# Kernel optimization log

Hardware: AMD Instinct MI355X
Metric: run time of the kernel (lower is better)

The kernel has to match this reference:

```python
import jax, jax.numpy as jnp
import numpy as np

S, B, H = 2048, 16, 512      # seq_len, batch, hidden_size
L = 4096                     # total labels across batch
SMAX = 16                    # max span length
LAB = 256                    # label_size
V = 32000                    # len(voc)


def setup_inputs() -> dict:
    key = jax.random.key(0)
    ks = jax.random.split(key, 10)
    hidden = jax.random.normal(ks[0], (S, B, H), jnp.float32)
    begins = jax.random.randint(ks[1], (L,), 1, S - SMAX - 1)          # >=1 so begin-1 valid
    lens = jax.random.randint(ks[2], (L,), 1, SMAX + 1)                # span length in [1, SMAX]
    ends = begins + lens                                               # < S so hidden[end] valid
    bids = jax.random.randint(ks[3], (L,), 0, B)
    tags = jax.random.randint(ks[4], (L,), 0, V)
    sc = 0.02
    W1 = jax.random.normal(ks[5], (3 * H, LAB), jnp.float32) * sc
    b1 = jnp.zeros((LAB,), jnp.float32)
    W2 = jax.random.normal(ks[6], (LAB, LAB), jnp.float32) * sc
    b2 = jnp.zeros((LAB,), jnp.float32)
    Wo = jax.random.normal(ks[7], (LAB, V), jnp.float32) * sc
    bo = jnp.zeros((V,), jnp.float32)
    return dict(hidden=hidden, begins=begins, ends=ends, bids=bids, tags=tags,
                W1=W1, b1=b1, W2=W2, b2=b2, Wo=Wo, bo=bo)


def reference(hidden, begins, ends, bids, tags, W1, b1, W2, b2, Wo, bo):
    # --- batched span embed: gather + masked mean + boundary concat ---
    pos = begins[:, None] + jnp.arange(SMAX)            # [L, SMAX]
    valid = (pos < ends[:, None]).astype(hidden.dtype)  # [L, SMAX]
    posc = jnp.minimum(pos, S - 1)
    g = hidden[posc, bids[:, None]]                     # [L, SMAX, H] gather
    span_len = (ends - begins).astype(hidden.dtype)[:, None]
    mean = (g * valid[..., None]).sum(axis=1) / span_len           # [L, H]
    left = hidden[begins - 1, bids]                                 # [L, H]
    right = hidden[ends, bids]                                      # [L, H]
    span_emb = jnp.concatenate([left, mean, right], axis=-1)        # [L, 3H]
    # --- hidden2feature: Linear -> sigmoid -> Linear (dropout = eval identity) ---
    feat = jax.nn.sigmoid(span_emb @ W1 + b1) @ W2 + b2             # [L, LAB]
    # --- SoftmaxLoss: -log_softmax(h2o(feat)).gather(tags).mean() per label ---
    logp = jax.nn.log_softmax(feat @ Wo + bo, axis=-1)              # [L, V]
    per_label = -logp[jnp.arange(L), tags]                          # one tag per label
    return per_label.sum() / (L + 1e-5)
```

## Files before the change

### kernel.cpp

```cpp
#include <hip/hip_runtime.h>
#include <math.h>

#define S 2048
#define B 16
#define H 512
#define L 4096
#define SMAX 16
#define LAB 256
#define V 32000
#define NCH 250
#define LOG2E 1.44269504f

typedef __attribute__((ext_vector_type(8))) short short8;
typedef __attribute__((ext_vector_type(4))) float float4v;

__device__ inline ushort f2bf(float x) {
  union { float f; unsigned u; } c; c.f = x;
  unsigned r = c.u + 0x7fffu + ((c.u >> 16) & 1u);
  return (ushort)(r >> 16);
}
__device__ inline float bf2f(ushort h) {
  union { unsigned u; float f; } c; c.u = ((unsigned)h) << 16;
  return c.f;
}

__global__ __launch_bounds__(256) void prep_kernel(
    const float* __restrict__ hidden, const int* __restrict__ begins,
    const int* __restrict__ ends, const int* __restrict__ bids,
    ushort* __restrict__ spanb, const float* __restrict__ W1,
    ushort* __restrict__ W1b, const float* __restrict__ W2,
    ushort* __restrict__ W2b, const float* __restrict__ Wo,
    ushort* __restrict__ Wob) {
  __shared__ ushort tile[64 * 72];
  int bid = blockIdx.x;
  int t = threadIdx.x;

  if (bid < 2048) {
    int sub = t >> 7, tt = t & 127;
    int l = bid * 2 + sub;
    int b = bids[l], s0 = begins[l], s1 = ends[l];
    const float4* hidv = (const float4*)hidden;
    float4 lf = hidv[((size_t)(s0 - 1) * B + b) * 128 + tt];
    float4 rf = hidv[((size_t)s1 * B + b) * 128 + tt];
    float4 m = make_float4(0.f, 0.f, 0.f, 0.f);
    int len = s1 - s0;
    for (int j = 0; j < len; ++j) {
      float4 g = hidv[((size_t)(s0 + j) * B + b) * 128 + tt];
      m.x += g.x; m.y += g.y; m.z += g.z; m.w += g.w;
    }
    float inv = 1.0f / (float)len;
    ushort* sp = spanb + (size_t)l * 1536;
    ushort4 u;
    u.x = f2bf(lf.x); u.y = f2bf(lf.y); u.z = f2bf(lf.z); u.w = f2bf(lf.w);
    *(ushort4*)&sp[tt * 4] = u;
    u.x = f2bf(m.x * inv); u.y = f2bf(m.y * inv);
    u.z = f2bf(m.z * inv); u.w = f2bf(m.w * inv);
    *(ushort4*)&sp[512 + tt * 4] = u;
    u.x = f2bf(rf.x); u.y = f2bf(rf.y); u.z = f2bf(rf.z); u.w = f2bf(rf.w);
    *(ushort4*)&sp[1024 + tt * 4] = u;
    return;
  }

  const float* src; ushort* dst; int K, N, n0, k0; bool wo = false;
  if (bid < 2144) {
    int u = bid - 2048; src = W1; dst = W1b; K = 1536; N = 256;
    n0 = (u & 3) * 64; k0 = (u >> 2) * 64;
  } else if (bid < 2160) {
    int u = bid - 2144; src = W2; dst = W2b; K = 256; N = 256;
    n0 = (u & 3) * 64; k0 = (u >> 2) * 64;
  } else {
    int u = bid - 2160; src = Wo; dst = Wob; K = 256; N = V;
    n0 = (u % 500) * 64; k0 = (u / 500) * 64; wo = true;
  }
  #pragma unroll
  for (int p = 0; p < 16; ++p) {
    int k = p * 4 + (t >> 6);
    int n = t & 63;
    tile[n * 72 + k] = f2bf(src[(size_t)(k0 + k) * N + n0 + n]);
  }
  __syncthreads();
  if (!wo) {
    #pragma unroll
    for (int p = 0; p < 2; ++p) {
      int idx = p * 256 + t;
      int n = idx >> 3, c = idx & 7;
      *(uint4*)&dst[(size_t)(n0 + n) * K + k0 + c * 8] =
          *(const uint4*)&tile[n * 72 + c * 8];
    }
  } else {
    #pragma unroll
    for (int p = 0; p < 2; ++p) {
      int idx = p * 256 + t;
      int n = idx >> 3, c8 = idx & 7;
      int v = n0 + n, k = k0 + c8 * 8;
      int c = v >> 7, nt = (v >> 4) & 7, lr = v & 15;
      int kh = k >> 7, k4 = (k >> 5) & 3, lq = (k >> 3) & 3;
      size_t f = ((((size_t)c * 2 + kh) * 4 + k4) * 8 + nt) * 64 + lq * 16 + lr;
      *(uint4*)&dst[f * 8] = *(const uint4*)&tile[n * 72 + c8 * 8];
    }
  }
}

__global__ __launch_bounds__(256) void feat_mfma_kernel(
    const ushort* __restrict__ spanb, const ushort* __restrict__ W1b,
    const float* __restrict__ b1, const ushort* __restrict__ W2b,
    const float* __restrict__ b2, ushort* __restrict__ featb,
    float* __restrict__ out) {
  __shared__ ushort Hs[16 * 264];
  int tid = threadIdx.x;
  if (blockIdx.x == 0 && tid == 0) *out = 0.f;
  int w = tid >> 6, lane = tid & 63;
  int lr = lane & 15, lq = lane >> 4;
  int l0 = blockIdx.x * 16;

  const short8* arow = (const short8*)(spanb + (size_t)(l0 + lr) * 1536 + lq * 8);
  const short8* brow[4];
  #pragma unroll
  for (int nt = 0; nt < 4; ++nt)
    brow[nt] = (const short8*)(W1b + (size_t)(w * 64 + nt * 16 + lr) * 1536 + lq * 8);

  float4v acc[4];
  float4v zero = {0.f, 0.f, 0.f, 0.f};
  #pragma unroll
  for (int nt = 0; nt < 4; ++nt) acc[nt] = zero;

  short8 af[2], bf[2][4];
  af[0] = arow[0];
  #pragma unroll
  for (int nt = 0; nt < 4; ++nt) bf[0][nt] = brow[nt][0];

  #pragma unroll
  for (int s = 0; s < 48; ++s) {
    int cur = s & 1, nxt = cur ^ 1;
    if (s < 47) {
      af[nxt] = arow[(s + 1) * 4];
      #pragma unroll
      for (int nt = 0; nt < 4; ++nt) bf[nxt][nt] = brow[nt][(s + 1) * 4];
    }
    #pragma unroll
    for (int nt = 0; nt < 4; ++nt)
      acc[nt] = __builtin_amdgcn_mfma_f32_16x16x32_bf16(
          af[cur], bf[cur][nt], acc[nt], 0, 0, 0);
  }

  {
    #pragma unroll
    for (int nt = 0; nt < 4; ++nt) {
      float b1v = b1[w * 64 + nt * 16 + lr];
      #pragma unroll
      for (int r = 0; r < 4; ++r) {
        int row = lq * 4 + r;
        float h = 1.0f / (1.0f + __expf(-(acc[nt][r] + b1v)));
        Hs[row * 264 + w * 64 + nt * 16 + lr] = f2bf(h);
      }
    }
  }
  __syncthreads();

  const short8* wrow[4];
  #pragma unroll
  for (int nt = 0; nt < 4; ++nt)
    wrow[nt] = (const short8*)(W2b + (size_t)(w * 64 + nt * 16 + lr) * 256 + lq * 8);

  float4v acc2[4];
  #pragma unroll
  for (int nt = 0; nt < 4; ++nt) acc2[nt] = zero;

  short8 bf2[2][4];
  #pragma unroll
  for (int nt = 0; nt < 4; ++nt) bf2[0][nt] = wrow[nt][0];

  #pragma unroll
  for (int s = 0; s < 8; ++s) {
    int cur = s & 1, nxt = cur ^ 1;
    if (s < 7) {
      #pragma unroll
      for (int nt = 0; nt < 4; ++nt) bf2[nxt][nt] = wrow[nt][(s + 1) * 4];
    }
    short8 af2 = *(const short8*)&Hs[lr * 264 + s * 32 + lq * 8];
    #pragma unroll
    for (int nt = 0; nt < 4; ++nt)
      acc2[nt] = __builtin_amdgcn_mfma_f32_16x16x32_bf16(
          af2, bf2[cur][nt], acc2[nt], 0, 0, 0);
  }

  {
    #pragma unroll
    for (int nt = 0; nt < 4; ++nt) {
      float b2v = b2[w * 64 + nt * 16 + lr];
      #pragma unroll
      for (int r = 0; r < 4; ++r) {
        int row = lq * 4 + r;
        int col = w * 64 + nt * 16 + lr;
        featb[(size_t)(l0 + row) * 256 + col] = f2bf(acc2[nt][r] + b2v);
      }
    }
  }
}

__global__ __launch_bounds__(256, 4) void logits_kernel(
    const ushort* __restrict__ featb, const ushort* __restrict__ Wob,
    const float* __restrict__ bo, const int* __restrict__ tags,
    float* __restrict__ pz, float* __restrict__ tagl) {
  __shared__ ushort Blds[16384];
  int bid = blockIdx.x;
  int tid = threadIdx.x;
  int lane = tid & 63;
  int lr = lane & 15, lq = lane >> 4;

  if (bid >= 4000) {
    int l = (bid - 4000) * 4 + (tid >> 6);
    int tg = tags[l];
    int c = tg >> 7, nt = (tg >> 4) & 7, tlr = tg & 15;
    int k0 = lane << 2;
    int kh = k0 >> 7, k4 = (k0 >> 5) & 3, tlq = (k0 >> 3) & 3, e = k0 & 7;
    size_t f = ((((size_t)c * 2 + kh) * 4 + k4) * 8 + nt) * 64 + tlq * 16 + tlr;
    ushort4 wa = *(const ushort4*)&Wob[f * 8 + e];
    ushort4 fa = *(const ushort4*)&featb[(size_t)l * 256 + k0];
    float s = bf2f(fa.x) * bf2f(wa.x) + bf2f(fa.y) * bf2f(wa.y) +
              bf2f(fa.z) * bf2f(wa.z) + bf2f(fa.w) * bf2f(wa.w);
    #pragma unroll
    for (int off = 1; off < 64; off <<= 1) s += __shfl_xor(s, off);
    if (lane == 0) tagl[l] = s + bo[tg];
    return;
  }

  int w = tid >> 6;
  int lb = bid & 31;
  int cpair = bid >> 5;
  int c0 = cpair * 2, c1 = c0 + 1;
  int l0 = lb * 128;

  const short8* aptr[2];
  #pragma unroll
  for (int mt = 0; mt < 2; ++mt)
    aptr[mt] = (const short8*)(featb +
        (size_t)(l0 + w * 32 + mt * 16 + lr) * 256 + lq * 8);

  float4v acc[2][8];
  float4v zero = {0.f, 0.f, 0.f, 0.f};
  #pragma unroll
  for (int mt = 0; mt < 2; ++mt)
    #pragma unroll
    for (int nt = 0; nt < 8; ++nt) acc[mt][nt] = zero;

  short8 af[2][2];
  #pragma unroll
  for (int mt = 0; mt < 2; ++mt) af[0][mt] = aptr[mt][0];

#define STAGE_HALF(ch, kh)                                                    \
  {                                                                           \
    const uint4* src4 = (const uint4*)(Wob +                                  \
        (size_t)(ch) * 32768 + (size_t)(kh) * 16384);                         \
    _Pragma("unroll")                                                         \
    for (int p = 0; p < 8; ++p) {                                             \
      int idx = p * 256 + tid;                                                \
      __builtin_amdgcn_global_load_lds(                                       \
          (const __attribute__((address_space(1))) unsigned int*)(src4 + idx),\
          (__attribute__((address_space(3))) unsigned int*)&Blds[(size_t)idx * 8], \
          16, 0, 0);                                                          \
    }                                                                         \
  }

#define KG_BLOCK(kh)                                                          \
  _Pragma("unroll")                                                           \
  for (int k4 = 0; k4 < 4; ++k4) {                                            \
    int kg = (kh) * 4 + k4;                                                   \
    int cur = kg & 1, nxt = cur ^ 1;                                          \
    if (kg < 7) {                                                             \
      _Pragma("unroll")                                                       \
      for (int mt = 0; mt < 2; ++mt)                                          \
        af[nxt][mt] = aptr[mt][(kg + 1) * 4];                                 \
    }                                                                         \
    short8 bf[8];                                                             \
    _Pragma("unroll")                                                         \
    for (int nt = 0; nt < 8; ++nt)                                            \
      bf[nt] = *(const short8*)&Blds[(size_t)(((k4 * 8 + nt) * 64) + lane) * 8]; \
    __builtin_amdgcn_s_setprio(1);                                            \
    _Pragma("unroll")                                                         \
    for (int mt = 0; mt < 2; ++mt)                                            \
      _Pragma("unroll")                                                       \
      for (int nt = 0; nt < 8; ++nt)                                          \
        acc[mt][nt] = __builtin_amdgcn_mfma_f32_16x16x32_bf16(                \
            af[cur][mt], bf[nt], acc[mt][nt], 0, 0, 0);                       \
    __builtin_amdgcn_s_setprio(0);                                            \
  }

#define EPILOGUE(ch)                                                          \
  {                                                                           \
    float z[2][4];                                                            \
    _Pragma("unroll")                                                         \
    for (int mt = 0; mt < 2; ++mt)                                            \
      _Pragma("unroll")                                                       \
      for (int r = 0; r < 4; ++r) z[mt][r] = 0.f;                             \
    _Pragma("unroll")                                                         \
    for (int mt = 0; mt < 2; ++mt)                                            \
      _Pragma("unroll")                                                       \
      for (int nt = 0; nt < 8; ++nt)                                          \
        _Pragma("unroll")                                                     \
        for (int r = 0; r < 4; ++r)                                           \
          z[mt][r] += exp2f(fmaf(acc[mt][nt][r], LOG2E, bov[nt]));            \
    _Pragma("unroll")                                                         \
    for (int mt = 0; mt < 2; ++mt)                                            \
      _Pragma("unroll")                                                       \
      for (int r = 0; r < 4; ++r) {                                           \
        _Pragma("unroll")                                                     \
        for (int off = 1; off < 16; off <<= 1)                                \
          z[mt][r] += __shfl_xor(z[mt][r], off);                              \
      }                                                                       \
    if (lr == 0) {                                                            \
      _Pragma("unroll")                                                       \
      for (int mt = 0; mt < 2; ++mt) {                                        \
        float4 v4;                                                            \
        v4.x = z[mt][0]; v4.y = z[mt][1]; v4.z = z[mt][2]; v4.w = z[mt][3];   \
        *(float4*)&pz[(size_t)(ch) * L + l0 + w * 32 + mt * 16 + lq * 4] = v4;\
      }                                                                       \
    }                                                                         \
  }

  STAGE_HALF(c0, 0);
  __syncthreads();
  KG_BLOCK(0);
  __syncthreads();
  STAGE_HALF(c0, 1);
  __syncthreads();
  KG_BLOCK(1);

  float bov[8];
  #pragma unroll
  for (int nt = 0; nt < 8; ++nt)
    bov[nt] = bo[c0 * 128 + nt * 16 + lr] * LOG2E;
  #pragma unroll
  for (int mt = 0; mt < 2; ++mt) af[0][mt] = aptr[mt][0];
  __syncthreads();
  STAGE_HALF(c1, 0);
  EPILOGUE(c0);
  #pragma unroll
  for (int mt = 0; mt < 2; ++mt)
    #pragma unroll
    for (int nt = 0; nt < 8; ++nt) acc[mt][nt] = zero;
  __syncthreads();

  KG_BLOCK(0);
  __syncthreads();
  STAGE_HALF(c1, 1);
  __syncthreads();
  KG_BLOCK(1);
  #pragma unroll
  for (int nt = 0; nt < 8; ++nt)
    bov[nt] = bo[c1 * 128 + nt * 16 + lr] * LOG2E;
  EPILOGUE(c1);

#undef STAGE_HALF
#undef KG_BLOCK
#undef EPILOGUE
}

__global__ __launch_bounds__(256) void reduce_kernel(
    const float* __restrict__ pz, const float* __restrict__ tagl,
    float* __restrict__ out) {
  int l = blockIdx.x * 256 + threadIdx.x;
  float z = 0.f;
  for (int c = 0; c < NCH; ++c) z += pz[(size_t)c * L + l];
  float per = logf(z) - tagl[l];
  float v = per * (1.0f / (4096.0f + 1e-5f));
  #pragma unroll
  for (int off = 1; off < 64; off <<= 1) v += __shfl_xor(v, off);
  __shared__ float wsum[4];
  if ((threadIdx.x & 63) == 0) wsum[threadIdx.x >> 6] = v;
  __syncthreads();
  if (threadIdx.x == 0)
    atomicAdd(out, wsum[0] + wsum[1] + wsum[2] + wsum[3]);
}

extern "C" void kernel_launch(void* const* d_in, const int* in_sizes, int n_in,
                              void* d_out, int out_size, void* d_ws,
                              size_t ws_size, hipStream_t stream) {
  const float* hidden = (const float*)d_in[0];
  const int* begins = (const int*)d_in[1];
  const int* ends = (const int*)d_in[2];
  const int* bids = (const int*)d_in[3];
  const int* tags = (const int*)d_in[4];
  const float* W1 = (const float*)d_in[5];
  const float* b1 = (const float*)d_in[6];
  const float* W2 = (const float*)d_in[7];
  const float* b2 = (const float*)d_in[8];
  const float* Wo = (const float*)d_in[9];
  const float* bo = (const float*)d_in[10];
  float* out = (float*)d_out;

  ushort* featb = (ushort*)d_ws;
  ushort* Wob = featb + (size_t)L * 256;
  ushort* spanb = Wob + (size_t)V * 256;
  ushort* W1b = spanb + (size_t)L * 1536;
  ushort* W2b = W1b + (size_t)256 * 1536;
  float* pz = (float*)spanb;
  float* tagl = (float*)(W2b + (size_t)256 * 256);

  prep_kernel<<<4160, 256, 0, stream>>>(hidden, begins, ends, bids, spanb,
                                        W1, W1b, W2, W2b, Wo, Wob);
  feat_mfma_kernel<<<256, 256, 0, stream>>>(spanb, W1b, b1, W2b, b2, featb,
                                            out);
  logits_kernel<<<5024, 256, 0, stream>>>(featb, Wob, bo, tags, pz, tagl);
  reduce_kernel<<<L / 256, 256, 0, stream>>>(pz, tagl, out);
}
```

Before: 287.5 us.

## Restructure logits kernel to 512-thread blocks per vocab chunk with double-buffered LDS

The logits kernel now uses a 2D grid: one block per 256-row slab and per 128-wide vocab chunk, run by 8 waves instead of 4, with both K-halves of the Wo chunk staged into two LDS buffers up front. The second half's load overlaps with the first half's MFMAs, and the extra waves share the staged B tile. Previously each block handled two chunks in sequence with more barriers. The tag-logit gather moves into its own small kernel, and the reduce loop is partially unrolled. This adds a kernel launch and doubles LDS per block, which may limit occupancy.

```diff
diff --git a/kernel.cpp b/kernel.cpp
--- a/kernel.cpp
+++ b/kernel.cpp
@@ -198,38 +198,15 @@
   }
 }
 
-__global__ __launch_bounds__(256, 4) void logits_kernel(
+__global__ __launch_bounds__(512, 4) void logits2_kernel(
     const ushort* __restrict__ featb, const ushort* __restrict__ Wob,
-    const float* __restrict__ bo, const int* __restrict__ tags,
-    float* __restrict__ pz, float* __restrict__ tagl) {
-  __shared__ ushort Blds[16384];
-  int bid = blockIdx.x;
+    const float* __restrict__ bo, float* __restrict__ pz) {
+  __shared__ ushort Blds[2][16384];
   int tid = threadIdx.x;
-  int lane = tid & 63;
+  int w = tid >> 6, lane = tid & 63;
   int lr = lane & 15, lq = lane >> 4;
-
-  if (bid >= 4000) {
-    int l = (bid - 4000) * 4 + (tid >> 6);
-    int tg = tags[l];
-    int c = tg >> 7, nt = (tg >> 4) & 7, tlr = tg & 15;
-    int k0 = lane << 2;
-    int kh = k0 >> 7, k4 = (k0 >> 5) & 3, tlq = (k0 >> 3) & 3, e = k0 & 7;
-    size_t f = ((((size_t)c * 2 + kh) * 4 + k4) * 8 + nt) * 64 + tlq * 16 + tlr;
-    ushort4 wa = *(const ushort4*)&Wob[f * 8 + e];
-    ushort4 fa = *(const ushort4*)&featb[(size_t)l * 256 + k0];
-    float s = bf2f(fa.x) * bf2f(wa.x) + bf2f(fa.y) * bf2f(wa.y) +
-              bf2f(fa.z) * bf2f(wa.z) + bf2f(fa.w) * bf2f(wa.w);
-    #pragma unroll
-    for (int off = 1; off < 64; off <<= 1) s += __shfl_xor(s, off);
-    if (lane == 0) tagl[l] = s + bo[tg];
-    return;
-  }
-
-  int w = tid >> 6;
-  int lb = bid & 31;
-  int cpair = bid >> 5;
-  int c0 = cpair * 2, c1 = c0 + 1;
-  int l0 = lb * 128;
+  int l0 = blockIdx.x * 256;
+  int v0 = blockIdx.y * 128;
 
   const short8* aptr[2];
   #pragma unroll
@@ -248,21 +225,22 @@
   #pragma unroll
   for (int mt = 0; mt < 2; ++mt) af[0][mt] = aptr[mt][0];
 
-#define STAGE_HALF(ch, kh)                                                    \
+#define STAGE_HALF(buf, kh)                                                   \
   {                                                                           \
     const uint4* src4 = (const uint4*)(Wob +                                  \
-        (size_t)(ch) * 32768 + (size_t)(kh) * 16384);                         \
+        (size_t)blockIdx.y * 32768 + (size_t)(kh) * 16384);                   \
     _Pragma("unroll")                                                         \
-    for (int p = 0; p < 8; ++p) {                                             \
-      int idx = p * 256 + tid;                                                \
+    for (int p = 0; p < 4; ++p) {                                             \
+      int idx = p * 512 + tid;                                                \
       __builtin_amdgcn_global_load_lds(                                       \
           (const __attribute__((address_space(1))) unsigned int*)(src4 + idx),\
-          (__attribute__((address_space(3))) unsigned int*)&Blds[(size_t)idx * 8], \
+          (__attribute__((address_space(3))) unsigned int*)                   \
+              &Blds[buf][(size_t)idx * 8],                                    \
           16, 0, 0);                                                          \
     }                                                                         \
   }
 
-#define KG_BLOCK(kh)                                                          \
+#define KG_BLOCK(buf, kh)                                                     \
   _Pragma("unroll")                                                           \
   for (int k4 = 0; k4 < 4; ++k4) {                                            \
     int kg = (kh) * 4 + k4;                                                   \
@@ -275,7 +253,8 @@
     short8 bf[8];                                                             \
     _Pragma("unroll")                                                         \
     for (int nt = 0; nt < 8; ++nt)                                            \
-      bf[nt] = *(const short8*)&Blds[(size_t)(((k4 * 8 + nt) * 64) + lane) * 8]; \
+      bf[nt] = *(const short8*)                                               \
+          &Blds[buf][(size_t)(((k4 * 8 + nt) * 64) + lane) * 8];              \
     __builtin_amdgcn_s_setprio(1);                                            \
     _Pragma("unroll")                                                         \
     for (int mt = 0; mt < 2; ++mt)                                            \
@@ -286,74 +265,69 @@
     __builtin_amdgcn_s_setprio(0);                                            \
   }
 
-#define EPILOGUE(ch)                                                          \
-  {                                                                           \
-    float z[2][4];                                                            \
-    _Pragma("unroll")                                                         \
-    for (int mt = 0; mt < 2; ++mt)                                            \
-      _Pragma("unroll")                                                       \
-      for (int r = 0; r < 4; ++r) z[mt][r] = 0.f;                             \
-    _Pragma("unroll")                                                         \
-    for (int mt = 0; mt < 2; ++mt)                                            \
-      _Pragma("unroll")                                                       \
-      for (int nt = 0; nt < 8; ++nt)                                          \
-        _Pragma("unroll")                                                     \
-        for (int r = 0; r < 4; ++r)                                           \
-          z[mt][r] += exp2f(fmaf(acc[mt][nt][r], LOG2E, bov[nt]));            \
-    _Pragma("unroll")                                                         \
-    for (int mt = 0; mt < 2; ++mt)                                            \
-      _Pragma("unroll")                                                       \
-      for (int r = 0; r < 4; ++r) {                                           \
-        _Pragma("unroll")                                                     \
-        for (int off = 1; off < 16; off <<= 1)                                \
-          z[mt][r] += __shfl_xor(z[mt][r], off);                              \
-      }                                                                       \
-    if (lr == 0) {                                                            \
-      _Pragma("unroll")                                                       \
-      for (int mt = 0; mt < 2; ++mt) {                                        \
-        float4 v4;                                                            \
-        v4.x = z[mt][0]; v4.y = z[mt][1]; v4.z = z[mt][2]; v4.w = z[mt][3];   \
-        *(float4*)&pz[(size_t)(ch) * L + l0 + w * 32 + mt * 16 + lq * 4] = v4;\
-      }                                                                       \
-    }                                                                         \
-  }
-
-  STAGE_HALF(c0, 0);
-  __syncthreads();
-  KG_BLOCK(0);
-  __syncthreads();
-  STAGE_HALF(c0, 1);
-  __syncthreads();
-  KG_BLOCK(1);
-
-  float bov[8];
-  #pragma unroll
-  for (int nt = 0; nt < 8; ++nt)
-    bov[nt] = bo[c0 * 128 + nt * 16 + lr] * LOG2E;
-  #pragma unroll
-  for (int mt = 0; mt < 2; ++mt) af[0][mt] = aptr[mt][0];
-  __syncthreads();
-  STAGE_HALF(c1, 0);
-  EPILOGUE(c0);
-  #pragma unroll
-  for (int mt = 0; mt < 2; ++mt)
-    #pragma unroll
-    for (int nt = 0; nt < 8; ++nt) acc[mt][nt] = zero;
-  __syncthreads();
-
-  KG_BLOCK(0);
-  __syncthreads();
-  STAGE_HALF(c1, 1);
-  __syncthreads();
-  KG_BLOCK(1);
-  #pragma unroll
-  for (int nt = 0; nt < 8; ++nt)
-    bov[nt] = bo[c1 * 128 + nt * 16 + lr] * LOG2E;
-  EPILOGUE(c1);
+  STAGE_HALF(0, 0);
+  __syncthreads();
+  STAGE_HALF(1, 1);
+  KG_BLOCK(0, 0);
+  __syncthreads();
+  KG_BLOCK(1, 1);
 
 #undef STAGE_HALF
 #undef KG_BLOCK
-#undef EPILOGUE
+
+  float bov[8];
+  #pragma unroll
+  for (int nt = 0; nt < 8; ++nt)
+    bov[nt] = bo[v0 + nt * 16 + lr] * LOG2E;
+  float z[2][4];
+  #pragma unroll
+  for (int mt = 0; mt < 2; ++mt)
+    #pragma unroll
+    for (int r = 0; r < 4; ++r) z[mt][r] = 0.f;
+  #pragma unroll
+  for (int mt = 0; mt < 2; ++mt)
+    #pragma unroll
+    for (int nt = 0; nt < 8; ++nt)
+      #pragma unroll
+      for (int r = 0; r < 4; ++r)
+        z[mt][r] += exp2f(fmaf(acc[mt][nt][r], LOG2E, bov[nt]));
+  #pragma unroll
+  for (int mt = 0; mt < 2; ++mt)
+    #pragma unroll
+    for (int r = 0; r < 4; ++r) {
+      #pragma unroll
+      for (int off = 1; off < 16; off <<= 1)
+        z[mt][r] += __shfl_xor(z[mt][r], off);
+    }
+  if (lr == 0) {
+    int ch = blockIdx.y;
+    #pragma unroll
+    for (int mt = 0; mt < 2; ++mt) {
+      float4 v4;
+      v4.x = z[mt][0]; v4.y = z[mt][1]; v4.z = z[mt][2]; v4.w = z[mt][3];
+      *(float4*)&pz[(size_t)ch * L + l0 + w * 32 + mt * 16 + lq * 4] = v4;
+    }
+  }
+}
+
+__global__ __launch_bounds__(256) void tag_kernel(
+    const ushort* __restrict__ featb, const ushort* __restrict__ Wob,
+    const float* __restrict__ bo, const int* __restrict__ tags,
+    float* __restrict__ tagl) {
+  int l = blockIdx.x * 4 + (threadIdx.x >> 6);
+  int lane = threadIdx.x & 63;
+  int tg = tags[l];
+  int c = tg >> 7, nt = (tg >> 4) & 7, lr = tg & 15;
+  int k0 = lane << 2;
+  int kh = k0 >> 7, k4 = (k0 >> 5) & 3, lq = (k0 >> 3) & 3, e = k0 & 7;
+  size_t f = ((((size_t)c * 2 + kh) * 4 + k4) * 8 + nt) * 64 + lq * 16 + lr;
+  ushort4 wa = *(const ushort4*)&Wob[f * 8 + e];
+  ushort4 fa = *(const ushort4*)&featb[(size_t)l * 256 + k0];
+  float s = bf2f(fa.x) * bf2f(wa.x) + bf2f(fa.y) * bf2f(wa.y) +
+            bf2f(fa.z) * bf2f(wa.z) + bf2f(fa.w) * bf2f(wa.w);
+  #pragma unroll
+  for (int off = 1; off < 64; off <<= 1) s += __shfl_xor(s, off);
+  if (lane == 0) tagl[l] = s + bo[tg];
 }
 
 __global__ __launch_bounds__(256) void reduce_kernel(
@@ -361,6 +335,7 @@
     float* __restrict__ out) {
   int l = blockIdx.x * 256 + threadIdx.x;
   float z = 0.f;
+  #pragma unroll 5
   for (int c = 0; c < NCH; ++c) z += pz[(size_t)c * L + l];
   float per = logf(z) - tagl[l];
   float v = per * (1.0f / (4096.0f + 1e-5f));
@@ -401,6 +376,7 @@
                                         W1, W1b, W2, W2b, Wo, Wob);
   feat_mfma_kernel<<<256, 256, 0, stream>>>(spanb, W1b, b1, W2b, b2, featb,
                                             out);
-  logits_kernel<<<5024, 256, 0, stream>>>(featb, Wob, bo, tags, pz, tagl);
+  logits2_kernel<<<dim3(16, NCH), 512, 0, stream>>>(featb, Wob, bo, pz);
+  tag_kernel<<<L / 4, 256, 0, stream>>>(featb, Wob, bo, tags, tagl);
   reduce_kernel<<<L / 256, 256, 0, stream>>>(pz, tagl, out);
 }
```

New measurement: 282.2 us (median of 2 runs). Within noise of the previous version (-1.8%).
